# Kernel optimization log

Measured on AMD Instinct MI355X. Metric: run time of the kernel, lower is better.

## Reference

```python
import jax, jax.numpy as jnp
import numpy as np

FWD_W = 1.0
BWD_W = 1.0
EPS = 1e-12  # guard sqrt gradient at exact zero


def setup_inputs() -> dict:
    key = jax.random.key(0)
    k1, k2 = jax.random.split(key)
    pred = jax.random.normal(k1, (4, 8192, 3), dtype=jnp.float32)
    target = jax.random.normal(k2, (4, 8192, 3), dtype=jnp.float32)
    return {"pred": pred, "target": target}


def reference(pred, target):
    # pairwise Euclidean distances (torch.cdist, p=2): (B, N, M)
    sq = (jnp.sum(pred * pred, axis=-1)[:, :, None]
          + jnp.sum(target * target, axis=-1)[:, None, :]
          - 2.0 * jnp.einsum('bnd,bmd->bnm', pred, target))
    dist = jnp.sqrt(jnp.maximum(sq, EPS))
    forward_dist = jnp.min(dist, axis=2)   # (B, N): pred -> nearest target
    backward_dist = jnp.min(dist, axis=1)  # (B, M): target -> nearest pred
    total = FWD_W * jnp.sum(forward_dist, axis=1) + BWD_W * jnp.sum(backward_dist, axis=1)
    return jnp.mean(total)  # reduction='mean'
```

## Files before the change

kernel.cpp:

```cpp
#include <hip/hip_runtime.h>
#include <math.h>

#define BATCH   4
#define NPTS    8192
#define THREADS 256
#define NQTOT   (2 * BATCH * NPTS)
#define CHUNK   1024
#define TSPLIT  2
#define THALF   (NPTS / TSPLIT)
#define NCHUNKS (THALF / CHUNK)

typedef _Float16 h8  __attribute__((ext_vector_type(8)));
typedef float    f16v __attribute__((ext_vector_type(16)));

__global__ __launch_bounds__(THREADS)
void chamfer_transform(const float* __restrict__ pred,
                       const float* __restrict__ target,
                       h8* __restrict__ trans_lo,
                       h8* __restrict__ trans_hi)
{
    const int p   = blockIdx.x * THREADS + threadIdx.x;
    const int arr = p >> 15;
    const int pb  = p & 32767;

    const float* src = (arr ? target : pred) + (size_t)pb * 3;
    const float x = src[0], y = src[1], z = src[2];

    const _Float16 hx = (_Float16)x;  const float lxf = x - (float)hx;
    const _Float16 hy = (_Float16)y;  const float lyf = y - (float)hy;
    const _Float16 hz = (_Float16)z;  const float lzf = z - (float)hz;
    const _Float16 lx = (_Float16)lxf, ly = (_Float16)lyf, lz = (_Float16)lzf;

    const float tx = (float)hx + (float)lx;
    const float ty = (float)hy + (float)ly;
    const float tz = (float)hz + (float)lz;
    const float tt = fmaf(tx, tx, fmaf(ty, ty, tz * tz));
    const _Float16 tth = (_Float16)tt;
    const _Float16 ttl = (_Float16)(tt - (float)tth);

    const _Float16 n2 = (_Float16)(-2.0f);
    h8 lo = { n2 * hx, n2 * hy, n2 * hz, tth,
              n2 * hx, n2 * hy, n2 * hz, ttl };
    h8 hi = { n2 * lx, n2 * ly, n2 * lz, (_Float16)0.0f,
              (_Float16)0.0f, (_Float16)0.0f, (_Float16)0.0f, (_Float16)0.0f };

    trans_lo[p] = lo;
    trans_hi[p] = hi;
}

__global__ __launch_bounds__(THREADS, 4)
void chamfer_min_kernel(const float* __restrict__ pred,
                        const float* __restrict__ target,
                        const h8* __restrict__ trans_lo,
                        const h8* __restrict__ trans_hi,
                        float* __restrict__ partial)
{
    __shared__ uint4 slo[CHUNK];
    __shared__ uint4 shi[CHUNK];

    const int tid  = threadIdx.x;
    const int lane = tid & 63;
    const int wave = tid >> 6;
    const int n    = lane & 31;
    const int hi   = lane >> 5;

    const int bid = blockIdx.x;
    const int ts  = bid & 1;
    const int qg  = (bid >> 1) & 63;
    const int b   = (bid >> 7) & 3;
    const int dir = bid >> 9;

    const int  qtbase = qg * 128 + wave * 32;
    const int  tbase  = ts * THALF;
    const int  darr   = (dir == 0) ? 1 : 0;
    const float* qraw = ((dir == 0) ? pred : target) + (size_t)b * NPTS * 3;

    h8 afrag;
    {
        const float* qp = qraw + (size_t)(qtbase + n) * 3;
        const float x = qp[0], y = qp[1], z = qp[2];
        const _Float16 hx = (_Float16)x; const _Float16 lx = (_Float16)(x - (float)hx);
        const _Float16 hy = (_Float16)y; const _Float16 ly = (_Float16)(y - (float)hy);
        const _Float16 hz = (_Float16)z; const _Float16 lz = (_Float16)(z - (float)hz);
        const _Float16 one  = (_Float16)1.0f;
        const _Float16 zero = (_Float16)0.0f;
        if (hi == 0) afrag = (h8){hx, hy, hz, one, lx, ly, lz, one};
        else         afrag = (h8){hx, hy, hz, zero, zero, zero, zero, zero};
    }

    float mn[16];
    #pragma unroll
    for (int i = 0; i < 16; ++i) mn[i] = 3.0e38f;

    const size_t gbase = (size_t)(darr * 4 + b) * NPTS + tbase;
    const h8* bsrc = hi ? (const h8*)shi : (const h8*)slo;

    for (int c = 0; c < NCHUNKS; ++c) {
        const size_t cb = gbase + (size_t)c * CHUNK;
        #pragma unroll
        for (int r = 0; r < 4; ++r) {
            slo[r * THREADS + tid] = ((const uint4*)trans_lo)[cb + r * THREADS + tid];
            shi[r * THREADS + tid] = ((const uint4*)trans_hi)[cb + r * THREADS + tid];
        }
        __syncthreads();

        #pragma unroll 2
        for (int t = 0; t < CHUNK / 32; ++t) {
            const h8 bfrag = bsrc[t * 32 + n];
            f16v zc = {};
            const f16v d = __builtin_amdgcn_mfma_f32_32x32x16_f16(afrag, bfrag, zc, 0, 0, 0);
            #pragma unroll
            for (int i = 0; i < 16; ++i) mn[i] = fminf(mn[i], d[i]);
        }
        __syncthreads();
    }

    #pragma unroll
    for (int mask = 1; mask <= 16; mask <<= 1) {
        #pragma unroll
        for (int i = 0; i < 16; ++i)
            mn[i] = fminf(mn[i], __shfl_xor(mn[i], mask, 64));
    }

    if (n == 0) {
        float* dst = partial + (size_t)ts * NQTOT
                   + (size_t)(dir * 4 + b) * NPTS + qtbase;
        #pragma unroll
        for (int i = 0; i < 16; ++i) {
            const int row = (i & 3) + 8 * (i >> 2) + 4 * hi;
            dst[row] = mn[i];
        }
    }
}

__global__ __launch_bounds__(THREADS)
void chamfer_reduce1(const float* __restrict__ partial,
                     const float* __restrict__ pred,
                     const float* __restrict__ target,
                     float* __restrict__ bsum)
{
    const int tid = threadIdx.x;
    const int i   = blockIdx.x * THREADS + tid;

    const float m = fminf(partial[i], partial[NQTOT + i]);

    const int dir  = i >> 15;
    const int rest = i & 32767;
    const float* qp = ((dir == 0) ? pred : target) + (size_t)rest * 3;
    const float x = qp[0], y = qp[1], z = qp[2];
    const float qq = fmaf(x, x, fmaf(y, y, z * z));

    float acc = sqrtf(fmaxf(qq + m, 1e-12f));

    #pragma unroll
    for (int off = 32; off > 0; off >>= 1)
        acc += __shfl_down(acc, off, 64);

    __shared__ float wsum[4];
    if ((tid & 63) == 0) wsum[tid >> 6] = acc;
    __syncthreads();
    if (tid == 0) bsum[blockIdx.x] = wsum[0] + wsum[1] + wsum[2] + wsum[3];
}

__global__ __launch_bounds__(THREADS)
void chamfer_reduce2(const float* __restrict__ bsum,
                     float* __restrict__ out)
{
    const int tid = threadIdx.x;
    float v = bsum[tid];
    #pragma unroll
    for (int off = 32; off > 0; off >>= 1)
        v += __shfl_down(v, off, 64);

    __shared__ float wsum[4];
    if ((tid & 63) == 0) wsum[tid >> 6] = v;
    __syncthreads();
    if (tid == 0) out[0] = (wsum[0] + wsum[1] + wsum[2] + wsum[3]) * (1.0f / BATCH);
}

extern "C" void kernel_launch(void* const* d_in, const int* in_sizes, int n_in,
                              void* d_out, int out_size, void* d_ws, size_t ws_size,
                              hipStream_t stream)
{
    const float* pred   = (const float*)d_in[0];
    const float* target = (const float*)d_in[1];
    float* out          = (float*)d_out;

    h8*    trans_lo = (h8*)d_ws;
    h8*    trans_hi = (h8*)((char*)d_ws + (size_t)65536 * 16);
    float* partial  = (float*)((char*)d_ws + (size_t)131072 * 16);
    float* bsum     = partial + 2 * NQTOT;

    chamfer_transform<<<NQTOT / THREADS / 1, THREADS, 0, stream>>>(
        pred, target, trans_lo, trans_hi);

    chamfer_min_kernel<<<2 * BATCH * 64 * TSPLIT, THREADS, 0, stream>>>(
        pred, target, trans_lo, trans_hi, partial);

    chamfer_reduce1<<<NQTOT / THREADS, THREADS, 0, stream>>>(
        partial, pred, target, bsum);

    chamfer_reduce2<<<1, THREADS, 0, stream>>>(bsum, out);
}
```

Baseline: 81.65 us.

## Register-block two query tiles per wave, split targets four ways, use direct global-to-LDS loads

Each wave now holds two A fragments covering 64 queries and reuses every pair of LDS-loaded B fragments across four MFMAs, which halves LDS reads per MFMA. The target range is split into four parts instead of two, with half as many query groups, so the grid size stays the same and the reduce kernel now takes the min over four partial buffers. Chunk staging uses global_load_lds to skip the round trip through registers. The cost is a doubled accumulator register set, which may reduce occupancy, and a larger partial buffer.

```diff
diff --git a/kernel.cpp b/kernel.cpp
--- a/kernel.cpp
+++ b/kernel.cpp
@@ -6,12 +6,19 @@
 #define THREADS 256
 #define NQTOT   (2 * BATCH * NPTS)
 #define CHUNK   1024
-#define TSPLIT  2
+#define TSPLIT  4
 #define THALF   (NPTS / TSPLIT)
 #define NCHUNKS (THALF / CHUNK)
 
 typedef _Float16 h8  __attribute__((ext_vector_type(8)));
 typedef float    f16v __attribute__((ext_vector_type(16)));
+
+__device__ __forceinline__ void glds16(const void* g, void* l)
+{
+    __builtin_amdgcn_global_load_lds(
+        (const __attribute__((address_space(1))) unsigned int*)g,
+        (__attribute__((address_space(3))) unsigned int*)l, 16, 0, 0);
+}
 
 __global__ __launch_bounds__(THREADS)
 void chamfer_transform(const float* __restrict__ pred,
@@ -48,6 +55,18 @@
     trans_hi[p] = hi;
 }
 
+__device__ __forceinline__ h8 make_afrag(const float* __restrict__ qp, const int hi)
+{
+    const float x = qp[0], y = qp[1], z = qp[2];
+    const _Float16 hx = (_Float16)x; const _Float16 lx = (_Float16)(x - (float)hx);
+    const _Float16 hy = (_Float16)y; const _Float16 ly = (_Float16)(y - (float)hy);
+    const _Float16 hz = (_Float16)z; const _Float16 lz = (_Float16)(z - (float)hz);
+    const _Float16 one  = (_Float16)1.0f;
+    const _Float16 zero = (_Float16)0.0f;
+    if (hi == 0) return (h8){hx, hy, hz, one, lx, ly, lz, one};
+    return (h8){hx, hy, hz, zero, zero, zero, zero, zero};
+}
+
 __global__ __launch_bounds__(THREADS, 4)
 void chamfer_min_kernel(const float* __restrict__ pred,
                         const float* __restrict__ target,
@@ -65,52 +84,53 @@
     const int hi   = lane >> 5;
 
     const int bid = blockIdx.x;
-    const int ts  = bid & 1;
-    const int qg  = (bid >> 1) & 63;
+    const int ts  = bid & 3;
+    const int qg  = (bid >> 2) & 31;
     const int b   = (bid >> 7) & 3;
     const int dir = bid >> 9;
 
-    const int  qtbase = qg * 128 + wave * 32;
+    const int  qtbase = qg * 256 + wave * 64;
     const int  tbase  = ts * THALF;
-    const int  darr   = (dir == 0) ? 1 : 0;
+    const int  darr   = dir ^ 1;
     const float* qraw = ((dir == 0) ? pred : target) + (size_t)b * NPTS * 3;
 
-    h8 afrag;
-    {
-        const float* qp = qraw + (size_t)(qtbase + n) * 3;
-        const float x = qp[0], y = qp[1], z = qp[2];
-        const _Float16 hx = (_Float16)x; const _Float16 lx = (_Float16)(x - (float)hx);
-        const _Float16 hy = (_Float16)y; const _Float16 ly = (_Float16)(y - (float)hy);
-        const _Float16 hz = (_Float16)z; const _Float16 lz = (_Float16)(z - (float)hz);
-        const _Float16 one  = (_Float16)1.0f;
-        const _Float16 zero = (_Float16)0.0f;
-        if (hi == 0) afrag = (h8){hx, hy, hz, one, lx, ly, lz, one};
-        else         afrag = (h8){hx, hy, hz, zero, zero, zero, zero, zero};
-    }
-
-    float mn[16];
-    #pragma unroll
-    for (int i = 0; i < 16; ++i) mn[i] = 3.0e38f;
+    const h8 afrag0 = make_afrag(qraw + (size_t)(qtbase + n) * 3, hi);
+    const h8 afrag1 = make_afrag(qraw + (size_t)(qtbase + 32 + n) * 3, hi);
+
+    float mn0[16], mn1[16];
+    #pragma unroll
+    for (int i = 0; i < 16; ++i) { mn0[i] = 3.0e38f; mn1[i] = 3.0e38f; }
 
     const size_t gbase = (size_t)(darr * 4 + b) * NPTS + tbase;
     const h8* bsrc = hi ? (const h8*)shi : (const h8*)slo;
+    const f16v zc = {};
 
     for (int c = 0; c < NCHUNKS; ++c) {
         const size_t cb = gbase + (size_t)c * CHUNK;
         #pragma unroll
         for (int r = 0; r < 4; ++r) {
-            slo[r * THREADS + tid] = ((const uint4*)trans_lo)[cb + r * THREADS + tid];
-            shi[r * THREADS + tid] = ((const uint4*)trans_hi)[cb + r * THREADS + tid];
+            glds16(((const uint4*)trans_lo) + cb + r * THREADS + tid,
+                   &slo[r * THREADS + tid]);
+            glds16(((const uint4*)trans_hi) + cb + r * THREADS + tid,
+                   &shi[r * THREADS + tid]);
         }
         __syncthreads();
 
-        #pragma unroll 2
-        for (int t = 0; t < CHUNK / 32; ++t) {
-            const h8 bfrag = bsrc[t * 32 + n];
-            f16v zc = {};
-            const f16v d = __builtin_amdgcn_mfma_f32_32x32x16_f16(afrag, bfrag, zc, 0, 0, 0);
+        for (int tp = 0; tp < CHUNK / 64; ++tp) {
+            const h8 b0 = bsrc[tp * 64 + n];
+            const h8 b1 = bsrc[tp * 64 + 32 + n];
+
+            const f16v d00 = __builtin_amdgcn_mfma_f32_32x32x16_f16(afrag0, b0, zc, 0, 0, 0);
+            const f16v d01 = __builtin_amdgcn_mfma_f32_32x32x16_f16(afrag0, b1, zc, 0, 0, 0);
             #pragma unroll
-            for (int i = 0; i < 16; ++i) mn[i] = fminf(mn[i], d[i]);
+            for (int i = 0; i < 16; ++i)
+                mn0[i] = fminf(fminf(d00[i], d01[i]), mn0[i]);
+
+            const f16v d10 = __builtin_amdgcn_mfma_f32_32x32x16_f16(afrag1, b0, zc, 0, 0, 0);
+            const f16v d11 = __builtin_amdgcn_mfma_f32_32x32x16_f16(afrag1, b1, zc, 0, 0, 0);
+            #pragma unroll
+            for (int i = 0; i < 16; ++i)
+                mn1[i] = fminf(fminf(d10[i], d11[i]), mn1[i]);
         }
         __syncthreads();
     }
@@ -118,8 +138,10 @@
     #pragma unroll
     for (int mask = 1; mask <= 16; mask <<= 1) {
         #pragma unroll
-        for (int i = 0; i < 16; ++i)
-            mn[i] = fminf(mn[i], __shfl_xor(mn[i], mask, 64));
+        for (int i = 0; i < 16; ++i) {
+            mn0[i] = fminf(mn0[i], __shfl_xor(mn0[i], mask, 64));
+            mn1[i] = fminf(mn1[i], __shfl_xor(mn1[i], mask, 64));
+        }
     }
 
     if (n == 0) {
@@ -128,7 +150,8 @@
         #pragma unroll
         for (int i = 0; i < 16; ++i) {
             const int row = (i & 3) + 8 * (i >> 2) + 4 * hi;
-            dst[row] = mn[i];
+            dst[row]      = mn0[i];
+            dst[32 + row] = mn1[i];
         }
     }
 }
@@ -142,7 +165,9 @@
     const int tid = threadIdx.x;
     const int i   = blockIdx.x * THREADS + tid;
 
-    const float m = fminf(partial[i], partial[NQTOT + i]);
+    const float m01 = fminf(partial[i],                 partial[NQTOT + i]);
+    const float m23 = fminf(partial[2 * NQTOT + i],     partial[3 * NQTOT + i]);
+    const float m   = fminf(m01, m23);
 
     const int dir  = i >> 15;
     const int rest = i & 32767;
@@ -189,12 +214,12 @@
     h8*    trans_lo = (h8*)d_ws;
     h8*    trans_hi = (h8*)((char*)d_ws + (size_t)65536 * 16);
     float* partial  = (float*)((char*)d_ws + (size_t)131072 * 16);
-    float* bsum     = partial + 2 * NQTOT;
-
-    chamfer_transform<<<NQTOT / THREADS / 1, THREADS, 0, stream>>>(
+    float* bsum     = partial + (size_t)TSPLIT * NQTOT;
+
+    chamfer_transform<<<NQTOT / THREADS, THREADS, 0, stream>>>(
         pred, target, trans_lo, trans_hi);
 
-    chamfer_min_kernel<<<2 * BATCH * 64 * TSPLIT, THREADS, 0, stream>>>(
+    chamfer_min_kernel<<<2 * BATCH * 32 * TSPLIT, THREADS, 0, stream>>>(
         pred, target, trans_lo, trans_hi, partial);
 
     chamfer_reduce1<<<NQTOT / THREADS, THREADS, 0, stream>>>(
```

Result: slower. 85.55 us (+4.8%).
